# Optimization experiments

Measured on AMD Instinct MI355X. Metric: run time of the kernel, lower is better.

## Reference

```python
import jax, jax.numpy as jnp
import numpy as np

B = 131072
IN_FEATS = 32
STATE = 128


def setup_inputs() -> dict:
    key = jax.random.key(0)
    k1, k2, k3, k4, k5 = jax.random.split(key, 5)
    stdv = 1.0 / np.sqrt(STATE)
    return {
        "input": jax.random.normal(k1, (B, IN_FEATS), dtype=jnp.float32),
        "old_h": jax.random.normal(k2, (B, STATE), dtype=jnp.float32),
        "old_cell": jax.random.normal(k3, (B, STATE), dtype=jnp.float32),
        "weights": jax.random.uniform(k4, (3 * STATE, IN_FEATS + STATE), dtype=jnp.float32, minval=-stdv, maxval=stdv),
        "bias": jax.random.uniform(k5, (3 * STATE,), dtype=jnp.float32, minval=-stdv, maxval=stdv),
    }


def reference(input, old_h, old_cell, weights, bias):
    # X: [B, state+in_feats] (old_h first, matching torch.cat([old_h, input], 1))
    X = jnp.concatenate([old_h, input], axis=1)
    # gate_weights: [B, 3*state] = X @ W^T + b (F.linear semantics)
    gate_weights = jnp.einsum('bf,gf->bg', X, weights) + bias
    ig_pre, og_pre, cc_pre = jnp.split(gate_weights, 3, axis=1)
    input_gate = jax.nn.sigmoid(ig_pre)
    output_gate = jax.nn.sigmoid(og_pre)
    candidate_cell = jax.nn.elu(cc_pre)
    new_cell = old_cell + candidate_cell * input_gate
    new_h = jnp.tanh(new_cell) * output_gate
    return (new_h, new_cell)
```

## Files before the change

kernel.cpp:

```cpp
#include <hip/hip_runtime.h>

#define TOTAL_B   131072
#define IN_FEATS  32
#define STATE     128
#define KDIM      160
#define BROWS     64
#define THREADS   512
#define LDSROW    384
#define GRID      512
#define ITERS     ((TOTAL_B / BROWS) / GRID)

typedef __bf16 bf16x8 __attribute__((ext_vector_type(8)));
typedef float  f32x4  __attribute__((ext_vector_type(4)));

__device__ __forceinline__ float fsigmoid(float x) { return 1.0f / (1.0f + __expf(-x)); }
__device__ __forceinline__ float ftanh(float x)    { return 2.0f / (1.0f + __expf(-2.0f * x)) - 1.0f; }

struct Xregs {
    f32x4 hlo[2], hhi[2];
    f32x4 xlo, xhi;
};

__device__ __forceinline__ void issue_x(const float* __restrict__ old_h,
                                        const float* __restrict__ xin,
                                        long b0, int t, Xregs& r)
{
    #pragma unroll
    for (int i = 0; i < 2; ++i) {
        int c   = t + i * THREADS;
        int row = c >> 4;
        int kc  = (c & 15) * 8;
        const float* p = old_h + (b0 + row) * (long)STATE + kc;
        r.hlo[i] = *(const f32x4*)p;
        r.hhi[i] = *((const f32x4*)p + 1);
    }
    if (t < 256) {
        int row = t >> 2;
        int kc  = (t & 3) * 8;
        const float* p = xin + (b0 + row) * (long)IN_FEATS + kc;
        r.xlo = *(const f32x4*)p;
        r.xhi = *((const f32x4*)p + 1);
    }
}

__device__ __forceinline__ void write_x(char* smem, int t, const Xregs& r)
{
    #pragma unroll
    for (int i = 0; i < 2; ++i) {
        int c   = t + i * THREADS;
        int row = c >> 4;
        int kc  = (c & 15) * 8;
        bf16x8 v;
        #pragma unroll
        for (int j = 0; j < 4; ++j) { v[j] = (__bf16)r.hlo[i][j]; v[j + 4] = (__bf16)r.hhi[i][j]; }
        int off = row * LDSROW + kc * 2;
        off ^= (row & 7) << 4;
        *(bf16x8*)(smem + off) = v;
    }
    if (t < 256) {
        int row = t >> 2;
        int kc  = (t & 3) * 8;
        bf16x8 v;
        #pragma unroll
        for (int j = 0; j < 4; ++j) { v[j] = (__bf16)r.xlo[j]; v[j + 4] = (__bf16)r.xhi[j]; }
        int off = row * LDSROW + (STATE + kc) * 2;
        off ^= (row & 7) << 4;
        *(bf16x8*)(smem + off) = v;
    }
}

__global__ __launch_bounds__(THREADS, 2) void lltm_fused(
    const float* __restrict__ xin,
    const float* __restrict__ old_h,
    const float* __restrict__ old_cell,
    const float* __restrict__ Wt,
    const float* __restrict__ bias,
    float* __restrict__ out)
{
    __shared__ __align__(128) char smem[2][BROWS * LDSROW];

    const int t    = threadIdx.x;
    const int lane = t & 63;
    const int wv   = t >> 6;
    const int l15  = lane & 15;
    const int lg   = lane >> 4;
    const int sbase = 16 * wv + 4 * lg;

    bf16x8 afrag[3][5];
    {
        const int g_lo = 16 * wv + l15;
        #pragma unroll
        for (int gt = 0; gt < 3; ++gt) {
            #pragma unroll
            for (int ks = 0; ks < 5; ++ks) {
                const float* p = Wt + (size_t)(gt * STATE + g_lo) * KDIM + ks * 32 + lg * 8;
                f32x4 lo = *(const f32x4*)p;
                f32x4 hi = *(const f32x4*)(p + 4);
                bf16x8 a;
                #pragma unroll
                for (int i = 0; i < 4; ++i) { a[i] = (__bf16)lo[i]; a[i + 4] = (__bf16)hi[i]; }
                afrag[gt][ks] = a;
            }
        }
    }
    const f32x4 b_ig = *(const f32x4*)(bias + sbase);
    const f32x4 b_og = *(const f32x4*)(bias + STATE + sbase);
    const f32x4 b_cc = *(const f32x4*)(bias + 2 * STATE + sbase);

    Xregs xr[2];
    issue_x(old_h, xin, (long)blockIdx.x * BROWS, t, xr[0]);

    #pragma unroll
    for (int it = 0; it < ITERS; ++it) {
        const long b0 = ((long)blockIdx.x + (long)it * GRID) * BROWS;

        f32x4 oc[4];
        #pragma unroll
        for (int sub = 0; sub < 4; ++sub)
            oc[sub] = *(const f32x4*)(old_cell + (b0 + sub * 16 + l15) * (long)STATE + sbase);

        write_x(smem[it & 1], t, xr[it & 1]);

        if (it + 1 < ITERS)
            issue_x(old_h, xin, ((long)blockIdx.x + (long)(it + 1) * GRID) * BROWS,
                    t, xr[(it + 1) & 1]);

        asm volatile("s_waitcnt lgkmcnt(0)\n\ts_barrier" ::: "memory");

        const char* sbuf = smem[it & 1];
        #pragma unroll
        for (int sub = 0; sub < 4; ++sub) {
            const int brow = sub * 16 + l15;
            f32x4 acc_ig = {0.f, 0.f, 0.f, 0.f};
            f32x4 acc_og = {0.f, 0.f, 0.f, 0.f};
            f32x4 acc_cc = {0.f, 0.f, 0.f, 0.f};
            #pragma unroll
            for (int ks = 0; ks < 5; ++ks) {
                int off = brow * LDSROW + (ks * 32 + lg * 8) * 2;
                off ^= (brow & 7) << 4;
                bf16x8 bfr = *(const bf16x8*)(sbuf + off);
                acc_ig = __builtin_amdgcn_mfma_f32_16x16x32_bf16(afrag[0][ks], bfr, acc_ig, 0, 0, 0);
                acc_og = __builtin_amdgcn_mfma_f32_16x16x32_bf16(afrag[1][ks], bfr, acc_og, 0, 0, 0);
                acc_cc = __builtin_amdgcn_mfma_f32_16x16x32_bf16(afrag[2][ks], bfr, acc_cc, 0, 0, 0);
            }
            const long bg = b0 + sub * 16 + l15;
            f32x4 nh, nc;
            #pragma unroll
            for (int j = 0; j < 4; ++j) {
                float ig = fsigmoid(acc_ig[j] + b_ig[j]);
                float og = fsigmoid(acc_og[j] + b_og[j]);
                float cp = acc_cc[j] + b_cc[j];
                float cc = cp > 0.f ? cp : (__expf(cp) - 1.0f);
                float c2 = oc[sub][j] + cc * ig;
                nc[j] = c2;
                nh[j] = ftanh(c2) * og;
            }
            __builtin_nontemporal_store(nh, (f32x4*)(out + bg * STATE + sbase));
            __builtin_nontemporal_store(nc, (f32x4*)(out + (long)TOTAL_B * STATE + bg * STATE + sbase));
        }
    }
}

extern "C" void kernel_launch(void* const* d_in, const int* in_sizes, int n_in,
                              void* d_out, int out_size, void* d_ws, size_t ws_size,
                              hipStream_t stream)
{
    const float* xin      = (const float*)d_in[0];
    const float* old_h    = (const float*)d_in[1];
    const float* old_cell = (const float*)d_in[2];
    const float* Wt       = (const float*)d_in[3];
    const float* bias     = (const float*)d_in[4];
    float* out = (float*)d_out;
    lltm_fused<<<GRID, THREADS, 0, stream>>>(xin, old_h, old_cell, Wt, bias, out);
}
```

Before: 67.51 us.

## Load input features directly into MFMA fragments, shrink LDS rows, raise occupancy

Stops staging the 32-wide input slice through LDS. Each lane now loads its input features from global memory straight into the last MFMA B-fragment, which shrinks the LDS row from 384 to 256 bytes. Launch bounds move from 2 to 3 blocks per CU, the first old_h prefetch is issued before the weight fragments load, and old_cell loads move after the barrier. The aim is less LDS traffic and footprint and more resident waves to hide memory latency. The cost is extra per-lane global loads that each wave issues redundantly across its 8 waves, plus tighter register pressure at the higher occupancy.

```diff
diff --git a/kernel.cpp b/kernel.cpp
--- a/kernel.cpp
+++ b/kernel.cpp
@@ -6,7 +6,7 @@
 #define KDIM      160
 #define BROWS     64
 #define THREADS   512
-#define LDSROW    384
+#define LDSROW    256
 #define GRID      512
 #define ITERS     ((TOTAL_B / BROWS) / GRID)
 
@@ -16,14 +16,10 @@
 __device__ __forceinline__ float fsigmoid(float x) { return 1.0f / (1.0f + __expf(-x)); }
 __device__ __forceinline__ float ftanh(float x)    { return 2.0f / (1.0f + __expf(-2.0f * x)) - 1.0f; }
 
-struct Xregs {
-    f32x4 hlo[2], hhi[2];
-    f32x4 xlo, xhi;
-};
+struct Hregs { f32x4 lo[2], hi[2]; };
 
-__device__ __forceinline__ void issue_x(const float* __restrict__ old_h,
-                                        const float* __restrict__ xin,
-                                        long b0, int t, Xregs& r)
+__device__ __forceinline__ void issue_h(const float* __restrict__ old_h,
+                                        long b0, int t, Hregs& r)
 {
     #pragma unroll
     for (int i = 0; i < 2; ++i) {
@@ -31,19 +27,12 @@
         int row = c >> 4;
         int kc  = (c & 15) * 8;
         const float* p = old_h + (b0 + row) * (long)STATE + kc;
-        r.hlo[i] = *(const f32x4*)p;
-        r.hhi[i] = *((const f32x4*)p + 1);
-    }
-    if (t < 256) {
-        int row = t >> 2;
-        int kc  = (t & 3) * 8;
-        const float* p = xin + (b0 + row) * (long)IN_FEATS + kc;
-        r.xlo = *(const f32x4*)p;
-        r.xhi = *((const f32x4*)p + 1);
+        r.lo[i] = *(const f32x4*)p;
+        r.hi[i] = *((const f32x4*)p + 1);
     }
 }
 
-__device__ __forceinline__ void write_x(char* smem, int t, const Xregs& r)
+__device__ __forceinline__ void write_h(char* smem, int t, const Hregs& r)
 {
     #pragma unroll
     for (int i = 0; i < 2; ++i) {
@@ -52,24 +41,14 @@
         int kc  = (c & 15) * 8;
         bf16x8 v;
         #pragma unroll
-        for (int j = 0; j < 4; ++j) { v[j] = (__bf16)r.hlo[i][j]; v[j + 4] = (__bf16)r.hhi[i][j]; }
+        for (int j = 0; j < 4; ++j) { v[j] = (__bf16)r.lo[i][j]; v[j + 4] = (__bf16)r.hi[i][j]; }
         int off = row * LDSROW + kc * 2;
-        off ^= (row & 7) << 4;
-        *(bf16x8*)(smem + off) = v;
-    }
-    if (t < 256) {
-        int row = t >> 2;
-        int kc  = (t & 3) * 8;
-        bf16x8 v;
-        #pragma unroll
-        for (int j = 0; j < 4; ++j) { v[j] = (__bf16)r.xlo[j]; v[j + 4] = (__bf16)r.xhi[j]; }
-        int off = row * LDSROW + (STATE + kc) * 2;
         off ^= (row & 7) << 4;
         *(bf16x8*)(smem + off) = v;
     }
 }
 
-__global__ __launch_bounds__(THREADS, 2) void lltm_fused(
+__global__ __launch_bounds__(THREADS, 3) void lltm_fused(
     const float* __restrict__ xin,
     const float* __restrict__ old_h,
     const float* __restrict__ old_cell,
@@ -85,6 +64,9 @@
     const int l15  = lane & 15;
     const int lg   = lane >> 4;
     const int sbase = 16 * wv + 4 * lg;
+
+    Hregs xr[2];
+    issue_h(old_h, (long)blockIdx.x * BROWS, t, xr[0]);
 
     bf16x8 afrag[3][5];
     {
@@ -107,43 +89,54 @@
     const f32x4 b_og = *(const f32x4*)(bias + STATE + sbase);
     const f32x4 b_cc = *(const f32x4*)(bias + 2 * STATE + sbase);
 
-    Xregs xr[2];
-    issue_x(old_h, xin, (long)blockIdx.x * BROWS, t, xr[0]);
-
     #pragma unroll
     for (int it = 0; it < ITERS; ++it) {
         const long b0 = ((long)blockIdx.x + (long)it * GRID) * BROWS;
+
+        write_h(smem[it & 1], t, xr[it & 1]);
+
+        if (it + 1 < ITERS)
+            issue_h(old_h, ((long)blockIdx.x + (long)(it + 1) * GRID) * BROWS,
+                    t, xr[(it + 1) & 1]);
+
+        asm volatile("s_waitcnt lgkmcnt(0)\n\ts_barrier" ::: "memory");
 
         f32x4 oc[4];
         #pragma unroll
         for (int sub = 0; sub < 4; ++sub)
             oc[sub] = *(const f32x4*)(old_cell + (b0 + sub * 16 + l15) * (long)STATE + sbase);
 
-        write_x(smem[it & 1], t, xr[it & 1]);
-
-        if (it + 1 < ITERS)
-            issue_x(old_h, xin, ((long)blockIdx.x + (long)(it + 1) * GRID) * BROWS,
-                    t, xr[(it + 1) & 1]);
-
-        asm volatile("s_waitcnt lgkmcnt(0)\n\ts_barrier" ::: "memory");
-
         const char* sbuf = smem[it & 1];
         #pragma unroll
         for (int sub = 0; sub < 4; ++sub) {
             const int brow = sub * 16 + l15;
+            const long bg  = b0 + brow;
+
+            const float* px = xin + bg * (long)IN_FEATS + lg * 8;
+            f32x4 xlo = *(const f32x4*)px;
+            f32x4 xhi = *((const f32x4*)px + 1);
+            bf16x8 bx;
+            #pragma unroll
+            for (int j = 0; j < 4; ++j) { bx[j] = (__bf16)xlo[j]; bx[j + 4] = (__bf16)xhi[j]; }
+
             f32x4 acc_ig = {0.f, 0.f, 0.f, 0.f};
             f32x4 acc_og = {0.f, 0.f, 0.f, 0.f};
             f32x4 acc_cc = {0.f, 0.f, 0.f, 0.f};
             #pragma unroll
             for (int ks = 0; ks < 5; ++ks) {
-                int off = brow * LDSROW + (ks * 32 + lg * 8) * 2;
-                off ^= (brow & 7) << 4;
-                bf16x8 bfr = *(const bf16x8*)(sbuf + off);
+                bf16x8 bfr;
+                if (ks < 4) {
+                    int off = brow * LDSROW + (ks * 32 + lg * 8) * 2;
+                    off ^= (brow & 7) << 4;
+                    bfr = *(const bf16x8*)(sbuf + off);
+                } else {
+                    bfr = bx;
+                }
                 acc_ig = __builtin_amdgcn_mfma_f32_16x16x32_bf16(afrag[0][ks], bfr, acc_ig, 0, 0, 0);
                 acc_og = __builtin_amdgcn_mfma_f32_16x16x32_bf16(afrag[1][ks], bfr, acc_og, 0, 0, 0);
                 acc_cc = __builtin_amdgcn_mfma_f32_16x16x32_bf16(afrag[2][ks], bfr, acc_cc, 0, 0, 0);
             }
-            const long bg = b0 + sub * 16 + l15;
+
             f32x4 nh, nc;
             #pragma unroll
             for (int j = 0; j < 4; ++j) {
```

After: 86.73 us. 28.5% more time.
